# Performance work log

Hardware: AMD Instinct MI355X
Metric: run time of the kernel (lower is better)

Reference implementation:

```python
import jax, jax.numpy as jnp
import numpy as np

N = 50000      # nodes
E = 600000     # edges
G = 512        # graphs in batch
H = 128        # hidden_dim
F_IN = 4       # node_features
ED = 2         # edge_dim
OUT = 256      # output_dim
L = 7          # conv layers 1..7 (layer 0 is separate: 4->128 with residual)
EPS = 1e-5     # BatchNorm eps


def setup_inputs() -> dict:
    key = jax.random.key(0)
    ks = jax.random.split(key, 32)
    rn = lambda k, shape, s=0.05: jax.random.normal(k, shape, dtype=jnp.float32) * s
    inp = {}
    inp["x"] = jax.random.normal(ks[0], (N, F_IN), dtype=jnp.float32)
    inp["edge_attr"] = jax.random.normal(ks[1], (E, ED), dtype=jnp.float32)
    # layer 0: EdgeUpdateConv(4, 128) with residual projection
    inp["We0"] = rn(ks[2], (F_IN + ED, H)); inp["be0"] = rn(ks[3], (H,))
    inp["Wn0"] = rn(ks[4], (H, H));        inp["bno0"] = rn(ks[5], (H,))
    inp["g0"] = jnp.ones((H,), jnp.float32); inp["bt0"] = jnp.zeros((H,), jnp.float32)
    inp["m0"] = rn(ks[6], (H,)); inp["v0"] = jax.random.uniform(ks[7], (H,), dtype=jnp.float32) + 0.5
    inp["Wr0"] = rn(ks[8], (F_IN, H)); inp["br0"] = rn(ks[9], (H,))
    # layers 1..7: EdgeUpdateConv(128, 128), stacked params
    inp["We_s"] = rn(ks[10], (L, H + ED, H)); inp["be_s"] = rn(ks[11], (L, H))
    inp["Wn_s"] = rn(ks[12], (L, H, H));      inp["bno_s"] = rn(ks[13], (L, H))
    inp["g_s"] = jnp.ones((L, H), jnp.float32); inp["bt_s"] = jnp.zeros((L, H), jnp.float32)
    inp["m_s"] = rn(ks[14], (L, H)); inp["v_s"] = jax.random.uniform(ks[15], (L, H), dtype=jnp.float32) + 0.5
    # head
    inp["W1"] = rn(ks[16], (2 * H, H)); inp["b1"] = rn(ks[17], (H,))
    inp["g1"] = jnp.ones((H,), jnp.float32); inp["bt1"] = jnp.zeros((H,), jnp.float32)
    inp["m1"] = rn(ks[18], (H,)); inp["v1"] = jax.random.uniform(ks[19], (H,), dtype=jnp.float32) + 0.5
    inp["W2"] = rn(ks[20], (H, OUT)); inp["b2"] = rn(ks[21], (OUT,))
    # int inputs
    inp["edge_index"] = jax.random.randint(ks[22], (2, E), 0, N, dtype=jnp.int32)
    inp["batch"] = jnp.sort(jax.random.randint(ks[23], (N,), 0, G, dtype=jnp.int32))
    return inp


def _bn(x, g, b, m, v):
    # eval-mode BatchNorm1d
    return (x - m) * (g * jax.lax.rsqrt(v + EPS)) + b


def reference(x, edge_attr, We0, be0, Wn0, bno0, g0, bt0, m0, v0, Wr0, br0,
              We_s, be_s, Wn_s, bno_s, g_s, bt_s, m_s, v_s,
              W1, b1, g1, bt1, m1, v1, W2, b2, edge_index, batch):
    src, dst = edge_index[0], edge_index[1]
    # in-degree for mean aggregation (isolated nodes -> 0 output, guard /0)
    deg = jnp.maximum(jax.ops.segment_sum(jnp.ones((E,), jnp.float32), dst, num_segments=N), 1.0)

    def conv(h, We, be, Wn, bno, g, bt, m, v, res):
        # message: gather x_j, concat edge_attr, linear_edge  -> [E, H]
        msg = jnp.concatenate([h[src], edge_attr], axis=1) @ We + be
        # scatter-mean aggregate -> [N, H]
        agg = jax.ops.segment_sum(msg, dst, num_segments=N) / deg[:, None]
        # update: linear_node, then BN, residual, ReLU
        out = _bn(agg @ Wn + bno, g, bt, m, v)
        return jax.nn.relu(out + res)

    h = conv(x, We0, be0, Wn0, bno0, g0, bt0, m0, v0, x @ Wr0 + br0)
    for i in range(L):  # fixed small layer loop
        h = conv(h, We_s[i], be_s[i], Wn_s[i], bno_s[i], g_s[i], bt_s[i], m_s[i], v_s[i], h)

    # global mean / max pooling per graph
    ones_n = jnp.ones((N,), jnp.float32)
    cnt = jnp.maximum(jax.ops.segment_sum(ones_n, batch, num_segments=G), 1.0)
    mean_p = jax.ops.segment_sum(h, batch, num_segments=G) / cnt[:, None]
    max_p = jax.ops.segment_max(h, batch, num_segments=G)
    z = jnp.concatenate([mean_p, max_p], axis=1)  # [G, 2H]
    z = jax.nn.relu(_bn(z @ W1 + b1, g1, bt1, m1, v1))
    z = z @ W2 + b2
    return z / jnp.maximum(jnp.linalg.norm(z, axis=1, keepdims=True), 1e-12)
```

## Files before the change

### kernel.cpp

```cpp
#include <hip/hip_runtime.h>
#include <hip/hip_bf16.h>

constexpr int NN   = 50000;
constexpr int NPAD = 50016;
constexpr int NE   = 600000;
constexpr int NG   = 512;
constexpr int HD   = 128;
constexpr float BN_EPS = 1e-5f;
constexpr int CWS  = HD*HD + 2*HD + HD;
constexpr int WMF_L = 2*4*4*128*8;

typedef __attribute__((ext_vector_type(8))) short bf16x8;
typedef __attribute__((ext_vector_type(4))) float f32x4;

__device__ inline unsigned short bf16rne(float v) {
  unsigned u = __float_as_uint(v);
  return (unsigned short)((u + 0x7FFFu + ((u >> 16) & 1u)) >> 16);
}
__device__ inline void bfsplit(float v, unsigned short& h, unsigned short& l) {
  unsigned short hb = bf16rne(v);
  float hf = __uint_as_float((unsigned)hb << 16);
  l = bf16rne(v - hf);
  h = hb;
}


__global__ __launch_bounds__(256) void k_deg(const int* __restrict__ ei,
                                             int* __restrict__ deg, int* __restrict__ rank) {
  int e = blockIdx.x * 256 + threadIdx.x;
  if (e >= NE) return;
  rank[e] = atomicAdd(&deg[ei[NE + e]], 1);
}

__global__ __launch_bounds__(1024) void k_scanA(const int* __restrict__ deg,
                                                int* __restrict__ rowptr, int* __restrict__ bsum) {
  __shared__ int sm[1024];
  int t = threadIdx.x, b = blockIdx.x;
  int i = b * 1024 + t;
  int v = (i < NN) ? deg[i] : 0;
  sm[t] = v;
  __syncthreads();
  for (int off = 1; off < 1024; off <<= 1) {
    int add = (t >= off) ? sm[t - off] : 0;
    __syncthreads();
    sm[t] += add;
    __syncthreads();
  }
  int incl = sm[t];
  if (i < NN) rowptr[i] = incl - v;
  if (t == 1023) bsum[b] = incl;
}

__global__ __launch_bounds__(1024) void k_scanC(int* rowptr, const int* __restrict__ bsum) {
  __shared__ int base;
  int b = blockIdx.x;
  if (threadIdx.x == 0) {
    int acc = 0;
    for (int j = 0; j < b; j++) acc += bsum[j];
    base = acc;
    if (b == 0) rowptr[NN] = NE;
  }
  __syncthreads();
  int i = b * 1024 + threadIdx.x;
  if (i < NN) rowptr[i] += base;
}

__global__ __launch_bounds__(256) void k_scatter(
    const int* __restrict__ ei, const float* __restrict__ ea, const int* __restrict__ rowptr,
    const int* __restrict__ rank, int* __restrict__ csr, float* __restrict__ eap) {
  int e = blockIdx.x * 256 + threadIdx.x;
  if (e >= NE) return;
  int s = ei[e], d = ei[NE + e];
  int pos = rowptr[d] + rank[e];
  csr[pos] = s;
  *(float2*)(eap + 2 * (size_t)pos) = *(const float2*)(ea + 2 * (size_t)e);
}

__global__ __launch_bounds__(256) void k_node_pre(
    const int* __restrict__ rowptr, const int* __restrict__ csr, const float* __restrict__ eap,
    const float* __restrict__ x, float* __restrict__ Sx, float* __restrict__ Se) {
  int i = blockIdx.x * 256 + threadIdx.x;
  if (i >= NN) return;
  int e0 = rowptr[i], e1 = rowptr[i + 1];
  float4 sx = make_float4(0.f, 0.f, 0.f, 0.f);
  float2 se = make_float2(0.f, 0.f);
  for (int e = e0; e < e1; e++) {
    int s = csr[e];
    float4 xv = *(const float4*)(x + 4 * (size_t)s);
    sx.x += xv.x; sx.y += xv.y; sx.z += xv.z; sx.w += xv.w;
    float2 ev = *(const float2*)(eap + 2 * (size_t)e);
    se.x += ev.x; se.y += ev.y;
  }
  *(float4*)(Sx + 4 * (size_t)i) = sx;
  *(float2*)(Se + 2 * (size_t)i) = se;
}

__global__ __launch_bounds__(128) void k_combine(
    const float* __restrict__ We0, const float* __restrict__ be0, const float* __restrict__ Wn0,
    const float* __restrict__ We_s, const float* __restrict__ be_s, const float* __restrict__ Wn_s,
    float* __restrict__ cw, unsigned short* __restrict__ wmf) {
  int l = blockIdx.x / 131;
  int r = blockIdx.x % 131;
  int j = threadIdx.x;
  float* slot = cw + (size_t)l * CWS;
  const float* Wn;
  const float* Arow;
  float* dst;
  if (l == 0) {
    Wn = Wn0;
    if (r < 4)       { Arow = We0 + r * HD; dst = slot + r * HD; }
    else if (r < 6)  { Arow = We0 + r * HD; dst = slot + HD * HD + (r - 4) * HD; }
    else if (r == 6) { Arow = be0;          dst = slot + HD * HD + 2 * HD; }
    else return;
  } else {
    int li = l - 1;
    Wn = Wn_s + (size_t)li * HD * HD;
    const float* We = We_s + (size_t)li * 130 * HD;
    if (r < 128)      { Arow = We + r * HD;  dst = slot + r * HD; }
    else if (r < 130) { Arow = We + r * HD;  dst = slot + HD * HD + (r - 128) * HD; }
    else              { Arow = be_s + li * HD; dst = slot + HD * HD + 2 * HD; }
  }
  float acc = 0.f;
  for (int t = 0; t < HD; t++) acc = fmaf(Arow[t], Wn[t * HD + j], acc);
  dst[j] = acc;
  if (l >= 1 && r < 128) {
    unsigned short hb, lb;
    bfsplit(acc, hb, lb);
    size_t wbase = (size_t)(l - 1) * WMF_L;
    int kb = r >> 5, ks2 = (r >> 3) & 3, jj = r & 7;
    size_t o = (size_t)((kb * 4 + ks2) * 128 + j) * 8 + jj;
    wmf[wbase + o] = hb;
    wmf[wbase + WMF_L / 2 + o] = lb;
  }
}


__global__ __launch_bounds__(256) void k_layer0(
    const float* __restrict__ x, const float* __restrict__ Sx, const float* __restrict__ Se,
    const int* __restrict__ deg, const float* __restrict__ cw0,
    const float* __restrict__ bno0, const float* __restrict__ g0, const float* __restrict__ bt0,
    const float* __restrict__ m0, const float* __restrict__ v0,
    const float* __restrict__ Wr0, const float* __restrict__ br0,
    float* __restrict__ outp, unsigned short* __restrict__ outbf) {
  int tid = threadIdx.x;
  int row = blockIdx.x * 2 + (tid >> 7);
  int c = tid & 127;
  const float* Wc0  = cw0;
  const float* wce0 = cw0 + HD * HD;
  const float* bc0  = cw0 + HD * HD + 2 * HD;
  float y = 0.f;
#pragma unroll
  for (int k = 0; k < 4; k++) y = fmaf(Sx[row * 4 + k], Wc0[k * HD + c], y);
  y = fmaf(Se[row * 2 + 0], wce0[c], y);
  y = fmaf(Se[row * 2 + 1], wce0[HD + c], y);
  float dg = (float)deg[row];
  y = fmaf(dg, bc0[c], y);
  float dgi = 1.0f / fmaxf(dg, 1.0f);
  y = y * dgi + bno0[c];
  float sc = g0[c] * rsqrtf(v0[c] + BN_EPS);
  float sh = bt0[c] - m0[c] * sc;
  y = y * sc + sh;
  float r = br0[c];
#pragma unroll
  for (int k = 0; k < 4; k++) r = fmaf(x[row * 4 + k], Wr0[k * HD + c], r);
  float o = fmaxf(y + r, 0.f);
  outp[(size_t)row * HD + c] = o;
  outbf[(size_t)row * HD + c] = bf16rne(o);
}


__global__ __launch_bounds__(256, 6) void k_layer(
    const float* __restrict__ h, const unsigned* __restrict__ hbf,
    const int* __restrict__ rowptr, const int* __restrict__ csr,
    const float* __restrict__ cwl, const unsigned short* __restrict__ wmf,
    const float* __restrict__ bno, const float* __restrict__ gam, const float* __restrict__ bet,
    const float* __restrict__ mu, const float* __restrict__ var,
    const float* __restrict__ Se, const int* __restrict__ deg,
    float* __restrict__ outp, unsigned short* __restrict__ outbf) {
  __shared__ unsigned short St_hi[32 * 136];
  __shared__ unsigned short St_lo[32 * 136];
  int tid = threadIdx.x;
  int wid = tid >> 6, lane = tid & 63;
  int half = lane >> 5, l5 = lane & 31;
  int rowbase = blockIdx.x * 32;
  const uint2* hb2 = (const uint2*)hbf;

#pragma unroll
  for (int r8 = 0; r8 < 8; r8++) {
    int lr = wid * 8 + r8;
    int i = __builtin_amdgcn_readfirstlane(rowbase + lr);
    float a0 = 0.f, a1 = 0.f, a2 = 0.f, a3 = 0.f;
    if (i < NN) {
      int e0 = rowptr[i], e1 = rowptr[i + 1];
      int e = e0 + half;
      for (; e + 6 < e1; e += 8) {
        int s0 = csr[e], s1 = csr[e + 2], s2 = csr[e + 4], s3 = csr[e + 6];
        uint2 v0 = hb2[(size_t)s0 * 32 + l5];
        uint2 v1 = hb2[(size_t)s1 * 32 + l5];
        uint2 v2 = hb2[(size_t)s2 * 32 + l5];
        uint2 v3 = hb2[(size_t)s3 * 32 + l5];
        a0 += __uint_as_float(v0.x << 16) + __uint_as_float(v1.x << 16)
            + __uint_as_float(v2.x << 16) + __uint_as_float(v3.x << 16);
        a1 += __uint_as_float(v0.x & 0xFFFF0000u) + __uint_as_float(v1.x & 0xFFFF0000u)
            + __uint_as_float(v2.x & 0xFFFF0000u) + __uint_as_float(v3.x & 0xFFFF0000u);
        a2 += __uint_as_float(v0.y << 16) + __uint_as_float(v1.y << 16)
            + __uint_as_float(v2.y << 16) + __uint_as_float(v3.y << 16);
        a3 += __uint_as_float(v0.y & 0xFFFF0000u) + __uint_as_float(v1.y & 0xFFFF0000u)
            + __uint_as_float(v2.y & 0xFFFF0000u) + __uint_as_float(v3.y & 0xFFFF0000u);
      }
      if (e + 2 < e1) {
        int s0 = csr[e], s1 = csr[e + 2];
        uint2 v0 = hb2[(size_t)s0 * 32 + l5];
        uint2 v1 = hb2[(size_t)s1 * 32 + l5];
        a0 += __uint_as_float(v0.x << 16) + __uint_as_float(v1.x << 16);
        a1 += __uint_as_float(v0.x & 0xFFFF0000u) + __uint_as_float(v1.x & 0xFFFF0000u);
        a2 += __uint_as_float(v0.y << 16) + __uint_as_float(v1.y << 16);
        a3 += __uint_as_float(v0.y & 0xFFFF0000u) + __uint_as_float(v1.y & 0xFFFF0000u);
        e += 4;
      }
      if (e < e1) {
        uint2 v = hb2[(size_t)csr[e] * 32 + l5];
        a0 += __uint_as_float(v.x << 16);
        a1 += __uint_as_float(v.x & 0xFFFF0000u);
        a2 += __uint_as_float(v.y << 16);
        a3 += __uint_as_float(v.y & 0xFFFF0000u);
      }
    }
    a0 += __shfl_xor(a0, 32);
    a1 += __shfl_xor(a1, 32);
    a2 += __shfl_xor(a2, 32);
    a3 += __shfl_xor(a3, 32);
    if (half == 0) {
      int o = lr * 136 + l5 * 4;
      unsigned short h0, l0, h1, l1, h2, l2, h3, l3;
      bfsplit(a0, h0, l0); bfsplit(a1, h1, l1);
      bfsplit(a2, h2, l2); bfsplit(a3, h3, l3);
      *(ushort4*)&St_hi[o] = make_ushort4(h0, h1, h2, h3);
      *(ushort4*)&St_lo[o] = make_ushort4(l0, l1, l2, l3);
    }
  }
  __syncthreads();

  int wm = wid >> 1, wn = wid & 1;
  int nlane = lane & 15, ksub = lane >> 4;
  const unsigned short* wh = wmf;
  const unsigned short* wl = wmf + WMF_L / 2;
  f32x4 acc[4];
#pragma unroll
  for (int nt = 0; nt < 4; nt++) acc[nt] = (f32x4){0.f, 0.f, 0.f, 0.f};
  int arow = wm * 16 + nlane;
#pragma unroll
  for (int ks = 0; ks < 4; ks++) {
    bf16x8 ah = *(const bf16x8*)&St_hi[arow * 136 + ks * 32 + ksub * 8];
    bf16x8 al = *(const bf16x8*)&St_lo[arow * 136 + ks * 32 + ksub * 8];
#pragma unroll
    for (int nt = 0; nt < 4; nt++) {
      int col = wn * 64 + nt * 16 + nlane;
      bf16x8 bh = *(const bf16x8*)&wh[(size_t)((ks * 4 + ksub) * 128 + col) * 8];
      bf16x8 bl = *(const bf16x8*)&wl[(size_t)((ks * 4 + ksub) * 128 + col) * 8];
      acc[nt] = __builtin_amdgcn_mfma_f32_16x16x32_bf16(ah, bh, acc[nt], 0, 0, 0);
      acc[nt] = __builtin_amdgcn_mfma_f32_16x16x32_bf16(al, bh, acc[nt], 0, 0, 0);
      acc[nt] = __builtin_amdgcn_mfma_f32_16x16x32_bf16(ah, bl, acc[nt], 0, 0, 0);
    }
  }

  const float* wce = cwl + HD * HD;
  const float* bcp = cwl + HD * HD + 2 * HD;
  int rb = wm * 16 + ksub * 4;
  float dgv[4], dgiv[4];
  float2 sevv[4];
#pragma unroll
  for (int i2 = 0; i2 < 4; i2++) {
    size_t row = (size_t)rowbase + rb + i2;
    float dg = (float)deg[row];
    dgv[i2] = dg;
    dgiv[i2] = 1.0f / fmaxf(dg, 1.0f);
    sevv[i2] = *(const float2*)(Se + row * 2);
  }
#pragma unroll
  for (int nt = 0; nt < 4; nt++) {
    int col = wn * 64 + nt * 16 + nlane;
    float w0 = wce[col], w1 = wce[HD + col], bcv = bcp[col], bnov = bno[col];
    float sc = gam[col] * rsqrtf(var[col] + BN_EPS);
    float sh = bet[col] - mu[col] * sc;
#pragma unroll
    for (int i2 = 0; i2 < 4; i2++) {
      size_t row = (size_t)rowbase + rb + i2;
      float y = (acc[nt][i2] + sevv[i2].x * w0 + sevv[i2].y * w1 + dgv[i2] * bcv) * dgiv[i2] + bnov;
      y = fmaxf(y * sc + sh + h[row * HD + col], 0.f);
      outp[row * HD + col] = y;
      outbf[row * HD + col] = bf16rne(y);
    }
  }
}


__global__ __launch_bounds__(512) void k_pool(
    const unsigned short* __restrict__ hb, const int* __restrict__ batch,
    float* __restrict__ meanp, float* __restrict__ maxp) {
  __shared__ float ssum[512], smax[512];
  int g = blockIdx.x, t = threadIdx.x;
  int d = t & 127, sub = t >> 7;
  int lo = 0, hi = NN;
  while (lo < hi) { int mid = (lo + hi) >> 1; if (batch[mid] < g) lo = mid + 1; else hi = mid; }
  int start = lo;
  lo = start; hi = NN;
  while (lo < hi) { int mid = (lo + hi) >> 1; if (batch[mid] < g + 1) lo = mid + 1; else hi = mid; }
  int end = lo;
  float sum = 0.f, mx = -3.4e38f;
  for (int i = start + sub; i < end; i += 4) {
    float val = __uint_as_float((unsigned)hb[(size_t)i * HD + d] << 16);
    sum += val;
    mx = fmaxf(mx, val);
  }
  ssum[t] = sum; smax[t] = mx;
  __syncthreads();
  if (sub == 0) {
    sum = ssum[t] + ssum[t + 128] + ssum[t + 256] + ssum[t + 384];
    mx = fmaxf(fmaxf(smax[t], smax[t + 128]), fmaxf(smax[t + 256], smax[t + 384]));
    int cnt = end - start;
    meanp[g * HD + d] = sum / fmaxf((float)cnt, 1.f);
    maxp[g * HD + d] = (cnt > 0) ? mx : 0.f;
  }
}

__global__ __launch_bounds__(256) void k_head(
    const float* __restrict__ meanp, const float* __restrict__ maxp,
    const float* __restrict__ W1, const float* __restrict__ b1,
    const float* __restrict__ g1, const float* __restrict__ bt1,
    const float* __restrict__ m1, const float* __restrict__ v1,
    const float* __restrict__ W2, const float* __restrict__ b2,
    float* __restrict__ outp) {
  __shared__ float z[256];
  __shared__ float s1[128];
  __shared__ float red[256];
  int g = blockIdx.x, t = threadIdx.x;
  z[t] = (t < 128) ? meanp[g * HD + t] : maxp[g * HD + (t - 128)];
  __syncthreads();
  if (t < 128) {
    float y = b1[t];
    for (int k = 0; k < 256; k++) y = fmaf(z[k], W1[k * HD + t], y);
    float sc = g1[t] * rsqrtf(v1[t] + BN_EPS);
    y = (y - m1[t]) * sc + bt1[t];
    s1[t] = fmaxf(y, 0.f);
  }
  __syncthreads();
  float o = b2[t];
  for (int k = 0; k < 128; k++) o = fmaf(s1[k], W2[k * 256 + t], o);
  red[t] = o * o;
  __syncthreads();
  for (int off = 128; off > 0; off >>= 1) {
    if (t < off) red[t] += red[t + off];
    __syncthreads();
  }
  float scale = 1.0f / fmaxf(sqrtf(red[0]), 1e-12f);
  outp[(size_t)g * 256 + t] = o * scale;
}


extern "C" void kernel_launch(void* const* d_in, const int* in_sizes, int n_in,
                              void* d_out, int out_size, void* d_ws, size_t ws_size,
                              hipStream_t stream) {
  const float* x         = (const float*)d_in[0];
  const float* edge_attr = (const float*)d_in[1];
  const float* We0  = (const float*)d_in[2];
  const float* be0  = (const float*)d_in[3];
  const float* Wn0  = (const float*)d_in[4];
  const float* bno0 = (const float*)d_in[5];
  const float* g0   = (const float*)d_in[6];
  const float* bt0  = (const float*)d_in[7];
  const float* m0   = (const float*)d_in[8];
  const float* v0   = (const float*)d_in[9];
  const float* Wr0  = (const float*)d_in[10];
  const float* br0  = (const float*)d_in[11];
  const float* We_s = (const float*)d_in[12];
  const float* be_s = (const float*)d_in[13];
  const float* Wn_s = (const float*)d_in[14];
  const float* bno_s= (const float*)d_in[15];
  const float* g_s  = (const float*)d_in[16];
  const float* bt_s = (const float*)d_in[17];
  const float* m_s  = (const float*)d_in[18];
  const float* v_s  = (const float*)d_in[19];
  const float* W1   = (const float*)d_in[20];
  const float* b1   = (const float*)d_in[21];
  const float* g1   = (const float*)d_in[22];
  const float* bt1  = (const float*)d_in[23];
  const float* m1   = (const float*)d_in[24];
  const float* v1   = (const float*)d_in[25];
  const float* W2   = (const float*)d_in[26];
  const float* b2   = (const float*)d_in[27];
  const int* edge_index = (const int*)d_in[28];
  const int* batch      = (const int*)d_in[29];
  float* outp = (float*)d_out;

  char* ws = (char*)d_ws;
  size_t off = 0;
  auto alloc = [&](size_t bytes) -> void* {
    void* p = ws + off;
    off = (off + bytes + 255) & ~(size_t)255;
    return p;
  };
  float* hA    = (float*)alloc((size_t)NPAD * HD * 4);
  float* hB    = (float*)alloc((size_t)NPAD * HD * 4);
  unsigned short* hAbf = (unsigned short*)alloc((size_t)NPAD * HD * 2);
  unsigned short* hBbf = (unsigned short*)alloc((size_t)NPAD * HD * 2);
  float* Sx    = (float*)alloc((size_t)NPAD * 4 * 4);
  float* Se    = (float*)alloc((size_t)NPAD * 2 * 4);
  int*   deg   = (int*)alloc((size_t)NPAD * 4);
  int*   rowptr= (int*)alloc((size_t)(NN + 1) * 4);
  int*   rank  = (int*)alloc((size_t)NE * 4);
  int*   csr   = (int*)alloc((size_t)NE * 4);
  float* eap   = (float*)alloc((size_t)NE * 2 * 4);
  int*   bsum  = (int*)alloc(64 * 4);
  float* cw    = (float*)alloc((size_t)8 * CWS * 4);
  unsigned short* wmf = (unsigned short*)alloc((size_t)7 * WMF_L * 2);
  float* meanp = (float*)alloc((size_t)NG * HD * 4);
  float* maxp  = (float*)alloc((size_t)NG * HD * 4);
  (void)ws_size; (void)n_in; (void)in_sizes; (void)out_size;

  hipMemsetAsync(deg, 0, (size_t)NPAD * 4, stream);
  hipMemsetAsync(Se, 0, (size_t)NPAD * 2 * 4, stream);

  k_deg<<<(NE + 255) / 256, 256, 0, stream>>>(edge_index, deg, rank);
  k_scanA<<<49, 1024, 0, stream>>>(deg, rowptr, bsum);
  k_scanC<<<49, 1024, 0, stream>>>(rowptr, bsum);
  k_scatter<<<(NE + 255) / 256, 256, 0, stream>>>(edge_index, edge_attr, rowptr, rank, csr, eap);
  k_node_pre<<<(NN + 255) / 256, 256, 0, stream>>>(rowptr, csr, eap, x, Sx, Se);
  k_combine<<<8 * 131, 128, 0, stream>>>(We0, be0, Wn0, We_s, be_s, Wn_s, cw, wmf);

  k_layer0<<<NN / 2, 256, 0, stream>>>(x, Sx, Se, deg, cw, bno0, g0, bt0, m0, v0, Wr0, br0,
                                       hA, hAbf);

  float* cur = hA;              float* oth = hB;
  unsigned short* curbf = hAbf; unsigned short* othbf = hBbf;
  for (int l = 1; l <= 7; ++l) {
    int li = l - 1;
    k_layer<<<NPAD / 32, 256, 0, stream>>>(cur, (const unsigned*)curbf, rowptr, csr,
        cw + (size_t)l * CWS, wmf + (size_t)li * WMF_L,
        bno_s + li * HD, g_s + li * HD, bt_s + li * HD, m_s + li * HD, v_s + li * HD,
        Se, deg, oth, othbf);
    float* t = cur; cur = oth; oth = t;
    unsigned short* tb = curbf; curbf = othbf; othbf = tb;
  }

  k_pool<<<NG, 512, 0, stream>>>(curbf, batch, meanp, maxp);
  k_head<<<NG, 256, 0, stream>>>(meanp, maxp, W1, b1, g1, bt1, m1, v1, W2, b2, outp);
}
```

Before: 591.0 us.

## Store hidden state as bf16 hi/lo split, interleave two-row gathers, warp-parallel node_pre

Replaces the fp32 hidden state plus bf16 copy with a bf16 hi/lo pair, so each layer writes 4 bytes per element instead of 6 and the residual is rebuilt from hi+lo. The gather loop now walks two destination rows at once to expose more independent loads, and the launch bounds raise the occupancy hint from 6 to 8. k_node_pre now gives each node 32 lanes plus a shuffle reduction instead of one thread per node. The cost is a slightly less exact residual (about 16 mantissa bits) and possible register pressure at the higher occupancy target.

```diff
diff --git a/kernel.cpp b/kernel.cpp
--- a/kernel.cpp
+++ b/kernel.cpp
@@ -23,6 +23,8 @@
   l = bf16rne(v - hf);
   h = hb;
 }
+__device__ inline float blo(unsigned u) { return __uint_as_float(u << 16); }
+__device__ inline float bhi(unsigned u) { return __uint_as_float(u & 0xFFFF0000u); }
 
 
 __global__ __launch_bounds__(256) void k_deg(const int* __restrict__ ei,
@@ -79,20 +81,29 @@
 __global__ __launch_bounds__(256) void k_node_pre(
     const int* __restrict__ rowptr, const int* __restrict__ csr, const float* __restrict__ eap,
     const float* __restrict__ x, float* __restrict__ Sx, float* __restrict__ Se) {
-  int i = blockIdx.x * 256 + threadIdx.x;
+  int g32 = threadIdx.x >> 5;
+  int i = blockIdx.x * 8 + g32;
   if (i >= NN) return;
+  int l = threadIdx.x & 31;
   int e0 = rowptr[i], e1 = rowptr[i + 1];
-  float4 sx = make_float4(0.f, 0.f, 0.f, 0.f);
-  float2 se = make_float2(0.f, 0.f);
-  for (int e = e0; e < e1; e++) {
+  float sx0 = 0.f, sx1 = 0.f, sx2 = 0.f, sx3 = 0.f, se0 = 0.f, se1 = 0.f;
+  for (int e = e0 + l; e < e1; e += 32) {
     int s = csr[e];
     float4 xv = *(const float4*)(x + 4 * (size_t)s);
-    sx.x += xv.x; sx.y += xv.y; sx.z += xv.z; sx.w += xv.w;
+    sx0 += xv.x; sx1 += xv.y; sx2 += xv.z; sx3 += xv.w;
     float2 ev = *(const float2*)(eap + 2 * (size_t)e);
-    se.x += ev.x; se.y += ev.y;
-  }
-  *(float4*)(Sx + 4 * (size_t)i) = sx;
-  *(float2*)(Se + 2 * (size_t)i) = se;
+    se0 += ev.x; se1 += ev.y;
+  }
+#pragma unroll
+  for (int m = 1; m <= 16; m <<= 1) {
+    sx0 += __shfl_xor(sx0, m); sx1 += __shfl_xor(sx1, m);
+    sx2 += __shfl_xor(sx2, m); sx3 += __shfl_xor(sx3, m);
+    se0 += __shfl_xor(se0, m); se1 += __shfl_xor(se1, m);
+  }
+  if (l == 0) {
+    *(float4*)(Sx + 4 * (size_t)i) = make_float4(sx0, sx1, sx2, sx3);
+    *(float2*)(Se + 2 * (size_t)i) = make_float2(se0, se1);
+  }
 }
 
 __global__ __launch_bounds__(128) void k_combine(
@@ -141,7 +152,7 @@
     const float* __restrict__ bno0, const float* __restrict__ g0, const float* __restrict__ bt0,
     const float* __restrict__ m0, const float* __restrict__ v0,
     const float* __restrict__ Wr0, const float* __restrict__ br0,
-    float* __restrict__ outp, unsigned short* __restrict__ outbf) {
+    unsigned short* __restrict__ outHi, unsigned short* __restrict__ outLo) {
   int tid = threadIdx.x;
   int row = blockIdx.x * 2 + (tid >> 7);
   int c = tid & 127;
@@ -164,79 +175,87 @@
 #pragma unroll
   for (int k = 0; k < 4; k++) r = fmaf(x[row * 4 + k], Wr0[k * HD + c], r);
   float o = fmaxf(y + r, 0.f);
-  outp[(size_t)row * HD + c] = o;
-  outbf[(size_t)row * HD + c] = bf16rne(o);
-}
-
-
-__global__ __launch_bounds__(256, 6) void k_layer(
-    const float* __restrict__ h, const unsigned* __restrict__ hbf,
+  unsigned short oh, ol;
+  bfsplit(o, oh, ol);
+  outHi[(size_t)row * HD + c] = oh;
+  outLo[(size_t)row * HD + c] = ol;
+}
+
+
+__global__ __launch_bounds__(256, 8) void k_layer(
+    const unsigned short* __restrict__ hHi, const unsigned short* __restrict__ hLo,
     const int* __restrict__ rowptr, const int* __restrict__ csr,
     const float* __restrict__ cwl, const unsigned short* __restrict__ wmf,
     const float* __restrict__ bno, const float* __restrict__ gam, const float* __restrict__ bet,
     const float* __restrict__ mu, const float* __restrict__ var,
     const float* __restrict__ Se, const int* __restrict__ deg,
-    float* __restrict__ outp, unsigned short* __restrict__ outbf) {
+    unsigned short* __restrict__ outHi, unsigned short* __restrict__ outLo) {
   __shared__ unsigned short St_hi[32 * 136];
   __shared__ unsigned short St_lo[32 * 136];
   int tid = threadIdx.x;
   int wid = tid >> 6, lane = tid & 63;
   int half = lane >> 5, l5 = lane & 31;
   int rowbase = blockIdx.x * 32;
-  const uint2* hb2 = (const uint2*)hbf;
-
-#pragma unroll
-  for (int r8 = 0; r8 < 8; r8++) {
-    int lr = wid * 8 + r8;
-    int i = __builtin_amdgcn_readfirstlane(rowbase + lr);
-    float a0 = 0.f, a1 = 0.f, a2 = 0.f, a3 = 0.f;
-    if (i < NN) {
-      int e0 = rowptr[i], e1 = rowptr[i + 1];
-      int e = e0 + half;
-      for (; e + 6 < e1; e += 8) {
-        int s0 = csr[e], s1 = csr[e + 2], s2 = csr[e + 4], s3 = csr[e + 6];
-        uint2 v0 = hb2[(size_t)s0 * 32 + l5];
-        uint2 v1 = hb2[(size_t)s1 * 32 + l5];
-        uint2 v2 = hb2[(size_t)s2 * 32 + l5];
-        uint2 v3 = hb2[(size_t)s3 * 32 + l5];
-        a0 += __uint_as_float(v0.x << 16) + __uint_as_float(v1.x << 16)
-            + __uint_as_float(v2.x << 16) + __uint_as_float(v3.x << 16);
-        a1 += __uint_as_float(v0.x & 0xFFFF0000u) + __uint_as_float(v1.x & 0xFFFF0000u)
-            + __uint_as_float(v2.x & 0xFFFF0000u) + __uint_as_float(v3.x & 0xFFFF0000u);
-        a2 += __uint_as_float(v0.y << 16) + __uint_as_float(v1.y << 16)
-            + __uint_as_float(v2.y << 16) + __uint_as_float(v3.y << 16);
-        a3 += __uint_as_float(v0.y & 0xFFFF0000u) + __uint_as_float(v1.y & 0xFFFF0000u)
-            + __uint_as_float(v2.y & 0xFFFF0000u) + __uint_as_float(v3.y & 0xFFFF0000u);
-      }
-      if (e + 2 < e1) {
-        int s0 = csr[e], s1 = csr[e + 2];
-        uint2 v0 = hb2[(size_t)s0 * 32 + l5];
-        uint2 v1 = hb2[(size_t)s1 * 32 + l5];
-        a0 += __uint_as_float(v0.x << 16) + __uint_as_float(v1.x << 16);
-        a1 += __uint_as_float(v0.x & 0xFFFF0000u) + __uint_as_float(v1.x & 0xFFFF0000u);
-        a2 += __uint_as_float(v0.y << 16) + __uint_as_float(v1.y << 16);
-        a3 += __uint_as_float(v0.y & 0xFFFF0000u) + __uint_as_float(v1.y & 0xFFFF0000u);
-        e += 4;
-      }
-      if (e < e1) {
-        uint2 v = hb2[(size_t)csr[e] * 32 + l5];
-        a0 += __uint_as_float(v.x << 16);
-        a1 += __uint_as_float(v.x & 0xFFFF0000u);
-        a2 += __uint_as_float(v.y << 16);
-        a3 += __uint_as_float(v.y & 0xFFFF0000u);
-      }
-    }
-    a0 += __shfl_xor(a0, 32);
-    a1 += __shfl_xor(a1, 32);
-    a2 += __shfl_xor(a2, 32);
-    a3 += __shfl_xor(a3, 32);
+  const uint2* hb2 = (const uint2*)hHi;
+
+#pragma unroll
+  for (int rp = 0; rp < 4; rp++) {
+    int lrA = wid * 8 + rp * 2, lrB = lrA + 1;
+    int iA = __builtin_amdgcn_readfirstlane(rowbase + lrA);
+    int iB = __builtin_amdgcn_readfirstlane(rowbase + lrB);
+    int eA = 0, eA1 = 0, eB = 0, eB1 = 0;
+    if (iA < NN) { eA = rowptr[iA] + half; eA1 = rowptr[iA + 1]; }
+    if (iB < NN) { eB = rowptr[iB] + half; eB1 = rowptr[iB + 1]; }
+    float A0 = 0.f, A1 = 0.f, A2 = 0.f, A3 = 0.f;
+    float B0 = 0.f, B1 = 0.f, B2 = 0.f, B3 = 0.f;
+    while ((eA + 2 < eA1) && (eB + 2 < eB1)) {
+      int sA0 = csr[eA], sA1 = csr[eA + 2], sB0 = csr[eB], sB1 = csr[eB + 2];
+      uint2 a0 = hb2[(size_t)sA0 * 32 + l5];
+      uint2 a1 = hb2[(size_t)sA1 * 32 + l5];
+      uint2 b0 = hb2[(size_t)sB0 * 32 + l5];
+      uint2 b1 = hb2[(size_t)sB1 * 32 + l5];
+      A0 += blo(a0.x) + blo(a1.x); A1 += bhi(a0.x) + bhi(a1.x);
+      A2 += blo(a0.y) + blo(a1.y); A3 += bhi(a0.y) + bhi(a1.y);
+      B0 += blo(b0.x) + blo(b1.x); B1 += bhi(b0.x) + bhi(b1.x);
+      B2 += blo(b0.y) + blo(b1.y); B3 += bhi(b0.y) + bhi(b1.y);
+      eA += 4; eB += 4;
+    }
+    while (eA + 2 < eA1) {
+      int s0 = csr[eA], s1 = csr[eA + 2];
+      uint2 a0 = hb2[(size_t)s0 * 32 + l5];
+      uint2 a1 = hb2[(size_t)s1 * 32 + l5];
+      A0 += blo(a0.x) + blo(a1.x); A1 += bhi(a0.x) + bhi(a1.x);
+      A2 += blo(a0.y) + blo(a1.y); A3 += bhi(a0.y) + bhi(a1.y);
+      eA += 4;
+    }
+    if (eA < eA1) {
+      uint2 a0 = hb2[(size_t)csr[eA] * 32 + l5];
+      A0 += blo(a0.x); A1 += bhi(a0.x); A2 += blo(a0.y); A3 += bhi(a0.y);
+    }
+    while (eB + 2 < eB1) {
+      int s0 = csr[eB], s1 = csr[eB + 2];
+      uint2 b0 = hb2[(size_t)s0 * 32 + l5];
+      uint2 b1 = hb2[(size_t)s1 * 32 + l5];
+      B0 += blo(b0.x) + blo(b1.x); B1 += bhi(b0.x) + bhi(b1.x);
+      B2 += blo(b0.y) + blo(b1.y); B3 += bhi(b0.y) + bhi(b1.y);
+      eB += 4;
+    }
+    if (eB < eB1) {
+      uint2 b0 = hb2[(size_t)csr[eB] * 32 + l5];
+      B0 += blo(b0.x); B1 += bhi(b0.x); B2 += blo(b0.y); B3 += bhi(b0.y);
+    }
+    A0 += __shfl_xor(A0, 32); A1 += __shfl_xor(A1, 32);
+    A2 += __shfl_xor(A2, 32); A3 += __shfl_xor(A3, 32);
+    B0 += __shfl_xor(B0, 32); B1 += __shfl_xor(B1, 32);
+    B2 += __shfl_xor(B2, 32); B3 += __shfl_xor(B3, 32);
     if (half == 0) {
-      int o = lr * 136 + l5 * 4;
       unsigned short h0, l0, h1, l1, h2, l2, h3, l3;
-      bfsplit(a0, h0, l0); bfsplit(a1, h1, l1);
-      bfsplit(a2, h2, l2); bfsplit(a3, h3, l3);
-      *(ushort4*)&St_hi[o] = make_ushort4(h0, h1, h2, h3);
-      *(ushort4*)&St_lo[o] = make_ushort4(l0, l1, l2, l3);
+      bfsplit(A0, h0, l0); bfsplit(A1, h1, l1); bfsplit(A2, h2, l2); bfsplit(A3, h3, l3);
+      *(ushort4*)&St_hi[lrA * 136 + l5 * 4] = make_ushort4(h0, h1, h2, h3);
+      *(ushort4*)&St_lo[lrA * 136 + l5 * 4] = make_ushort4(l0, l1, l2, l3);
+      bfsplit(B0, h0, l0); bfsplit(B1, h1, l1); bfsplit(B2, h2, l2); bfsplit(B3, h3, l3);
+      *(ushort4*)&St_hi[lrB * 136 + l5 * 4] = make_ushort4(h0, h1, h2, h3);
+      *(ushort4*)&St_lo[lrB * 136 + l5 * 4] = make_ushort4(l0, l1, l2, l3);
     }
   }
   __syncthreads();
@@ -286,10 +305,15 @@
 #pragma unroll
     for (int i2 = 0; i2 < 4; i2++) {
       size_t row = (size_t)rowbase + rb + i2;
+      size_t idx = row * HD + col;
+      float res = blo((unsigned)hHi[idx] << 16 >> 16 << 16) ;
+      res = __uint_as_float((unsigned)hHi[idx] << 16) + __uint_as_float((unsigned)hLo[idx] << 16);
       float y = (acc[nt][i2] + sevv[i2].x * w0 + sevv[i2].y * w1 + dgv[i2] * bcv) * dgiv[i2] + bnov;
-      y = fmaxf(y * sc + sh + h[row * HD + col], 0.f);
-      outp[row * HD + col] = y;
-      outbf[row * HD + col] = bf16rne(y);
+      y = fmaxf(y * sc + sh + res, 0.f);
+      unsigned short yh, yl;
+      bfsplit(y, yh, yl);
+      outHi[idx] = yh;
+      outLo[idx] = yl;
     }
   }
 }
@@ -400,10 +424,10 @@
     off = (off + bytes + 255) & ~(size_t)255;
     return p;
   };
-  float* hA    = (float*)alloc((size_t)NPAD * HD * 4);
-  float* hB    = (float*)alloc((size_t)NPAD * HD * 4);
-  unsigned short* hAbf = (unsigned short*)alloc((size_t)NPAD * HD * 2);
-  unsigned short* hBbf = (unsigned short*)alloc((size_t)NPAD * HD * 2);
+  unsigned short* hAHi = (unsigned short*)alloc((size_t)NPAD * HD * 2);
+  unsigned short* hALo = (unsigned short*)alloc((size_t)NPAD * HD * 2);
+  unsigned short* hBHi = (unsigned short*)alloc((size_t)NPAD * HD * 2);
+  unsigned short* hBLo = (unsigned short*)alloc((size_t)NPAD * HD * 2);
   float* Sx    = (float*)alloc((size_t)NPAD * 4 * 4);
   float* Se    = (float*)alloc((size_t)NPAD * 2 * 4);
   int*   deg   = (int*)alloc((size_t)NPAD * 4);
@@ -425,24 +449,25 @@
   k_scanA<<<49, 1024, 0, stream>>>(deg, rowptr, bsum);
   k_scanC<<<49, 1024, 0, stream>>>(rowptr, bsum);
   k_scatter<<<(NE + 255) / 256, 256, 0, stream>>>(edge_index, edge_attr, rowptr, rank, csr, eap);
-  k_node_pre<<<(NN + 255) / 256, 256, 0, stream>>>(rowptr, csr, eap, x, Sx, Se);
+  k_node_pre<<<(NN + 7) / 8, 256, 0, stream>>>(rowptr, csr, eap, x, Sx, Se);
   k_combine<<<8 * 131, 128, 0, stream>>>(We0, be0, Wn0, We_s, be_s, Wn_s, cw, wmf);
 
   k_layer0<<<NN / 2, 256, 0, stream>>>(x, Sx, Se, deg, cw, bno0, g0, bt0, m0, v0, Wr0, br0,
-                                       hA, hAbf);
-
-  float* cur = hA;              float* oth = hB;
-  unsigned short* curbf = hAbf; unsigned short* othbf = hBbf;
+                                       hAHi, hALo);
+
+  unsigned short* curHi = hAHi; unsigned short* curLo = hALo;
+  unsigned short* othHi = hBHi; unsigned short* othLo = hBLo;
   for (int l = 1; l <= 7; ++l) {
     int li = l - 1;
-    k_layer<<<NPAD / 32, 256, 0, stream>>>(cur, (const unsigned*)curbf, rowptr, csr,
+    k_layer<<<NPAD / 32, 256, 0, stream>>>(curHi, curLo, rowptr, csr,
         cw + (size_t)l * CWS, wmf + (size_t)li * WMF_L,
         bno_s + li * HD, g_s + li * HD, bt_s + li * HD, m_s + li * HD, v_s + li * HD,
-        Se, deg, oth, othbf);
-    float* t = cur; cur = oth; oth = t;
-    unsigned short* tb = curbf; curbf = othbf; othbf = tb;
-  }
-
-  k_pool<<<NG, 512, 0, stream>>>(curbf, batch, meanp, maxp);
+        Se, deg, othHi, othLo);
+    unsigned short* t;
+    t = curHi; curHi = othHi; othHi = t;
+    t = curLo; curLo = othLo; othLo = t;
+  }
+
+  k_pool<<<NG, 512, 0, stream>>>(curHi, batch, meanp, maxp);
   k_head<<<NG, 256, 0, stream>>>(meanp, maxp, W1, b1, g1, bt1, m1, v1, W2, b2, outp);
 }
```

Measured after the change: 560.3 us. 5.2% less time.
